# Performance work log

Hardware: AMD Instinct MI355X
Metric: run time of the kernel (lower is better)

## Reference

```python
import jax, jax.numpy as jnp
import numpy as np

LN_EPS = 1e-6


def setup_inputs() -> dict:
    key = jax.random.key(0)
    ks = jax.random.split(key, 3)
    B, S, L, H, V = 16, 512, 2, 1024, 32000
    x = jax.random.randint(ks[0], (B, S), 0, V, dtype=jnp.int64)
    embed = jax.random.normal(ks[1], (V, H), dtype=jnp.float32) * 0.02
    ln_gamma = jnp.ones((L, H), dtype=jnp.float32)
    ln_beta = jnp.zeros((L, H), dtype=jnp.float32)
    W = jax.random.normal(ks[2], (L, 2 * H, 4 * H), dtype=jnp.float32) * (1.0 / np.sqrt(2 * H))
    b = jnp.zeros((L, 4 * H), dtype=jnp.float32)
    return {"x": x, "embed": embed, "ln_gamma": ln_gamma, "ln_beta": ln_beta, "W": W, "b": b}


def _layer_norm(x, g, bt):
    mu = jnp.mean(x, axis=-1, keepdims=True)
    var = jnp.mean(jnp.square(x - mu), axis=-1, keepdims=True)
    return (x - mu) * jax.lax.rsqrt(var + LN_EPS) * g + bt


def reference(x, embed, ln_gamma, ln_beta, W, b):
    L, _, H4 = W.shape
    H = H4 // 4
    B, S = x.shape
    xe = embed[x]  # [B,S,H] token embedding (dropout is identity at eval)

    def step(carry, x_t):
        c, h = carry  # each [L,B,H]
        inp = x_t  # [B,H]
        cs, hs = [], []
        h_out = inp
        for m in range(L):
            xn = _layer_norm(inp, ln_gamma[m], ln_beta[m])
            z = jnp.concatenate([xn, h[m]], axis=-1) @ W[m] + b[m]  # [B,4H]
            zi, zf, zo, zg = z[:, :H], z[:, H:2 * H], z[:, 2 * H:3 * H], z[:, 3 * H:]
            c_new = jax.nn.sigmoid(zf) * c[m] + jax.nn.sigmoid(zi) * jnp.tanh(zg)
            h_new = jax.nn.sigmoid(zo) * jnp.tanh(c_new)
            cs.append(c_new)
            hs.append(h_new)
            h_out = h_new  # raw lstm output of top layer
            inp = h_new + inp  # residual connection feeds next layer
        return (jnp.stack(cs), jnp.stack(hs)), h_out

    c0 = jnp.zeros((L, B, H), dtype=xe.dtype)
    h0 = jnp.zeros((L, B, H), dtype=xe.dtype)
    (c_final, _), h_seq = jax.lax.scan(step, (c0, h0), jnp.transpose(xe, (1, 0, 2)))
    # h_seq: [S,B,H] -> tied-embedding logits [B,S,V]
    logits = jnp.einsum("sbh,vh->bsv", h_seq, embed)
    return c_final, logits
```

## Files before the change

kernel.cpp:

```cpp
#include <hip/hip_runtime.h>
#include <hip/hip_fp16.h>
#include <hip/hip_cooperative_groups.h>

namespace cg = cooperative_groups;

typedef _Float16 f16;
typedef _Float16 f16x8 __attribute__((ext_vector_type(8)));
typedef _Float16 f16x4 __attribute__((ext_vector_type(4)));
typedef float    f32x4 __attribute__((ext_vector_type(4)));

#define LN_EPS 1e-6f

__global__ void k_cvt(const float* __restrict__ in, f16* __restrict__ out, int n4) {
    int i = blockIdx.x * 256 + threadIdx.x;
    int st = gridDim.x * 256;
    for (; i < n4; i += st) {
        float4 v = ((const float4*)in)[i];
        f16x4 o = { (f16)v.x, (f16)v.y, (f16)v.z, (f16)v.w };
        ((f16x4*)out)[i] = o;
    }
}

__global__ void k_xstat(const int* __restrict__ x, const float* __restrict__ embed,
                        float2* __restrict__ xstat) {
    int r = blockIdx.x * 4 + (threadIdx.x >> 6);
    int lane = threadIdx.x & 63;
    int t = r >> 4, b = r & 15;
    int tok = x[b * 512 + t];
    const float4* p = (const float4*)(embed + (size_t)tok * 1024);
    float sum = 0.f, sq = 0.f;
    #pragma unroll
    for (int j = 0; j < 4; ++j) {
        float4 v = p[lane * 4 + j];
        sum += v.x + v.y + v.z + v.w;
        sq  += v.x*v.x + v.y*v.y + v.z*v.z + v.w*v.w;
    }
    #pragma unroll
    for (int m = 1; m < 64; m <<= 1) {
        sum += __shfl_xor(sum, m);
        sq  += __shfl_xor(sq,  m);
    }
    if (lane == 0) {
        float mu  = sum * (1.f / 1024.f);
        float var = sq  * (1.f / 1024.f) - mu * mu;
        xstat[r] = make_float2(mu, rsqrtf(var + LN_EPS));
    }
}

__global__ void __launch_bounds__(256, 1)
k_recur(const int* __restrict__ x, const float* __restrict__ embed,
        const float* __restrict__ gamma, const float* __restrict__ beta,
        const float* __restrict__ W, const float* __restrict__ bias,
        const float2* __restrict__ xstat,
        f16* __restrict__ h0buf, f16* __restrict__ h1buf,
        float* __restrict__ inp1buf,
        f16* __restrict__ hseq,
        float* __restrict__ cout)
{
    extern __shared__ char smem[];
    float* zred  = (float*)(smem + 131072);
    float* stats = (float*)(smem + 131072 + 8192);

    const int tid   = threadIdx.x;
    const int lane  = tid & 63;
    const int wv    = tid >> 6;
    const int blk   = blockIdx.x;
    const int layer = (blk < 128) ? 0 : 1;
    const int base  = (layer ? blk - 128 : blk) * 8;

    {
        const float* Wm = W + (size_t)layer * 2048 * 4096;
        for (int idx = tid; idx < 2048; idx += 256) {
            const int mat = idx >> 10;
            const int k   = idx & 1023;
            const float* row = Wm + (size_t)(mat * 1024 + k) * 4096 + base;
            #pragma unroll
            for (int g = 0; g < 4; ++g) {
                float4 a = *(const float4*)(row + g * 1024);
                float4 c = *(const float4*)(row + g * 1024 + 4);
                float vals[8] = {a.x, a.y, a.z, a.w, c.x, c.y, c.z, c.w};
                #pragma unroll
                for (int u = 0; u < 8; ++u) {
                    int lc  = g * 8 + u;
                    int off = (mat * 65536 + lc * 2048 + k * 2) ^ ((lc & 7) << 4);
                    *(f16*)(smem + off) = (f16)vals[u];
                }
            }
        }
    }

    int grow = 0, gcol = 0;
    float bz0 = 0, bz1 = 0, bz2 = 0, bz3 = 0;
    if (tid < 128) {
        grow = tid >> 3;
        gcol = base + (tid & 7);
        bz0 = bias[layer * 4096 + gcol];
        bz1 = bias[layer * 4096 + 1024 + gcol];
        bz2 = bias[layer * 4096 + 2048 + gcol];
        bz3 = bias[layer * 4096 + 3072 + gcol];
    }
    float creg = 0.f;

    const int arow = lane & 15;
    const int koff = (lane >> 4) * 8;
    const float* gam = gamma + layer * 1024;
    const float* bet = beta  + layer * 1024;

    cg::grid_group grid = cg::this_grid();
    __syncthreads();

    for (int tick = 0; tick <= 512; ++tick) {
        const int  step   = layer ? tick - 1 : tick;
        const bool active = layer ? (tick >= 1) : (tick < 512);
        if (active) {
            if (layer) {
                const float* ip = inp1buf + (step & 1) * (16 * 1024);
                int row = tid >> 4, seg = tid & 15;
                const float4* p = (const float4*)(ip + row * 1024 + seg * 64);
                float sum = 0.f, sq = 0.f;
                #pragma unroll
                for (int j = 0; j < 16; ++j) {
                    float4 v = p[j];
                    sum += v.x + v.y + v.z + v.w;
                    sq  += v.x*v.x + v.y*v.y + v.z*v.z + v.w*v.w;
                }
                #pragma unroll
                for (int m = 1; m < 16; m <<= 1) {
                    sum += __shfl_xor(sum, m);
                    sq  += __shfl_xor(sq,  m);
                }
                if (seg == 0) {
                    float mu  = sum * (1.f / 1024.f);
                    float var = sq  * (1.f / 1024.f) - mu * mu;
                    stats[row * 2]     = mu;
                    stats[row * 2 + 1] = rsqrtf(var + LN_EPS);
                }
                __syncthreads();
            }

            float mu, rsig;
            const float* xrow;
            const f16*   hrow;
            if (layer == 0) {
                int tok = x[arow * 512 + step];
                float2 st = xstat[step * 16 + arow];
                mu = st.x; rsig = st.y;
                xrow = embed + (size_t)tok * 1024;
                hrow = h0buf + ((step + 1) & 1) * (16 * 1024) + arow * 1024;
            } else {
                mu = stats[arow * 2]; rsig = stats[arow * 2 + 1];
                xrow = inp1buf + (step & 1) * (16 * 1024) + arow * 1024;
                hrow = h1buf + ((step + 1) & 1) * (16 * 1024) + arow * 1024;
            }

            f32x4 acc0 = {0.f, 0.f, 0.f, 0.f};
            f32x4 acc1 = {0.f, 0.f, 0.f, 0.f};
            const int lcA = lane & 15;
            #pragma unroll
            for (int ks = 0; ks < 8; ++ks) {
                const int k0 = wv * 256 + ks * 32 + koff;
                float4 e0 = *(const float4*)(xrow + k0);
                float4 e1 = *(const float4*)(xrow + k0 + 4);
                float4 g0 = *(const float4*)(gam + k0);
                float4 g1 = *(const float4*)(gam + k0 + 4);
                float4 q0 = *(const float4*)(bet + k0);
                float4 q1 = *(const float4*)(bet + k0 + 4);
                f16x8 xa;
                xa[0] = (f16)((e0.x - mu) * rsig * g0.x + q0.x);
                xa[1] = (f16)((e0.y - mu) * rsig * g0.y + q0.y);
                xa[2] = (f16)((e0.z - mu) * rsig * g0.z + q0.z);
                xa[3] = (f16)((e0.w - mu) * rsig * g0.w + q0.w);
                xa[4] = (f16)((e1.x - mu) * rsig * g1.x + q1.x);
                xa[5] = (f16)((e1.y - mu) * rsig * g1.y + q1.y);
                xa[6] = (f16)((e1.z - mu) * rsig * g1.z + q1.z);
                xa[7] = (f16)((e1.w - mu) * rsig * g1.w + q1.w);
                f16x8 ha = *(const f16x8*)(hrow + k0);

                int swz0 = (lcA * 2048 + k0 * 2) ^ ((lcA & 7) << 4);
                f16x8 wx0 = *(const f16x8*)(smem + swz0);
                f16x8 wh0 = *(const f16x8*)(smem + 65536 + swz0);
                acc0 = __builtin_amdgcn_mfma_f32_16x16x32_f16(xa, wx0, acc0, 0, 0, 0);
                acc0 = __builtin_amdgcn_mfma_f32_16x16x32_f16(ha, wh0, acc0, 0, 0, 0);
                int lc1  = 16 + lcA;
                int swz1 = (lc1 * 2048 + k0 * 2) ^ ((lc1 & 7) << 4);
                f16x8 wx1 = *(const f16x8*)(smem + swz1);
                f16x8 wh1 = *(const f16x8*)(smem + 65536 + swz1);
                acc1 = __builtin_amdgcn_mfma_f32_16x16x32_f16(xa, wx1, acc1, 0, 0, 0);
                acc1 = __builtin_amdgcn_mfma_f32_16x16x32_f16(ha, wh1, acc1, 0, 0, 0);
            }

            #pragma unroll
            for (int r = 0; r < 4; ++r) {
                int row = (lane >> 4) * 4 + r;
                zred[wv * 512 + row * 32 + (lane & 15)]      = acc0[r];
                zred[wv * 512 + row * 32 + 16 + (lane & 15)] = acc1[r];
            }
            __syncthreads();

            if (tid < 128) {
                int zb = grow * 32 + (tid & 7);
                float zi = bz0, zf = bz1, zo = bz2, zg = bz3;
                #pragma unroll
                for (int w = 0; w < 4; ++w) {
                    zi += zred[w * 512 + zb];
                    zf += zred[w * 512 + zb + 8];
                    zo += zred[w * 512 + zb + 16];
                    zg += zred[w * 512 + zb + 24];
                }
                float si = 1.f / (1.f + expf(-zi));
                float sf = 1.f / (1.f + expf(-zf));
                float so = 1.f / (1.f + expf(-zo));
                float cn = sf * creg + si * tanhf(zg);
                float hn = so * tanhf(cn);
                creg = cn;
                if (layer == 0) {
                    int tok = x[grow * 512 + step];
                    float xe = embed[(size_t)tok * 1024 + gcol];
                    inp1buf[(step & 1) * (16 * 1024) + grow * 1024 + gcol] = hn + xe;
                    h0buf[(step & 1) * (16 * 1024) + grow * 1024 + gcol]   = (f16)hn;
                } else {
                    h1buf[(step & 1) * (16 * 1024) + grow * 1024 + gcol]   = (f16)hn;
                    hseq[((size_t)step * 16 + grow) * 1024 + gcol]          = (f16)hn;
                }
            }
        }
        grid.sync();
    }

    if (tid < 128)
        cout[layer * (16 * 1024) + grow * 1024 + gcol] = creg;
}

__global__ void __launch_bounds__(256)
k_logits(const f16* __restrict__ A, const f16* __restrict__ Bm, float* __restrict__ out) {
    __shared__ f16 Asm[128 * 64];
    __shared__ f16 Bsm[128 * 64];
    const int nwg = gridDim.x;
    int swz = (blockIdx.x % 8) * (nwg / 8) + blockIdx.x / 8;
    const int tm = swz / 250;
    const int tn = swz % 250;
    const int tid = threadIdx.x;
    const int lane = tid & 63;
    const int wv = tid >> 6;
    const int wm = wv >> 1, wn = wv & 1;

    f32x4 acc[4][4] = {};
    const f16* Ab = A  + (size_t)(tm * 128) * 1024;
    const f16* Bb = Bm + (size_t)(tn * 128) * 1024;

    for (int kt = 0; kt < 16; ++kt) {
        uint4 ra[4], rb[4];
        #pragma unroll
        for (int j = 0; j < 4; ++j) {
            int c = tid + j * 256;
            int row = c >> 3, slot = c & 7;
            ra[j] = *(const uint4*)(Ab + (size_t)row * 1024 + kt * 64 + slot * 8);
            rb[j] = *(const uint4*)(Bb + (size_t)row * 1024 + kt * 64 + slot * 8);
        }
        __syncthreads();
        #pragma unroll
        for (int j = 0; j < 4; ++j) {
            int c = tid + j * 256;
            int row = c >> 3, slot = c & 7;
            int off = row * 128 + ((slot ^ (row & 7)) << 4);
            *(uint4*)((char*)Asm + off) = ra[j];
            *(uint4*)((char*)Bsm + off) = rb[j];
        }
        __syncthreads();
        #pragma unroll
        for (int ks = 0; ks < 2; ++ks) {
            f16x8 af[4], bf[4];
            #pragma unroll
            for (int mi = 0; mi < 4; ++mi) {
                int row = wm * 64 + mi * 16 + (lane & 15);
                int slot = ks * 4 + (lane >> 4);
                af[mi] = *(const f16x8*)((const char*)Asm + row * 128 + ((slot ^ (row & 7)) << 4));
            }
            #pragma unroll
            for (int ni = 0; ni < 4; ++ni) {
                int row = wn * 64 + ni * 16 + (lane & 15);
                int slot = ks * 4 + (lane >> 4);
                bf[ni] = *(const f16x8*)((const char*)Bsm + row * 128 + ((slot ^ (row & 7)) << 4));
            }
            #pragma unroll
            for (int mi = 0; mi < 4; ++mi)
                #pragma unroll
                for (int ni = 0; ni < 4; ++ni)
                    acc[mi][ni] = __builtin_amdgcn_mfma_f32_16x16x32_f16(af[mi], bf[ni], acc[mi][ni], 0, 0, 0);
        }
    }

    #pragma unroll
    for (int mi = 0; mi < 4; ++mi) {
        int m16 = tm * 128 + wm * 64 + mi * 16;
        int s = m16 >> 4;
        #pragma unroll
        for (int ni = 0; ni < 4; ++ni) {
            int v = tn * 128 + wn * 64 + ni * 16 + (lane & 15);
            #pragma unroll
            for (int r = 0; r < 4; ++r) {
                int b = (lane >> 4) * 4 + r;
                out[((size_t)b * 512 + s) * 32000 + v] = acc[mi][ni][r];
            }
        }
    }
}

extern "C" void kernel_launch(void* const* d_in, const int* in_sizes, int n_in,
                              void* d_out, int out_size, void* d_ws, size_t ws_size,
                              hipStream_t stream) {
    const int*   x     = (const int*)d_in[0];
    const float* embed = (const float*)d_in[1];
    const float* gamma = (const float*)d_in[2];
    const float* beta  = (const float*)d_in[3];
    const float* W     = (const float*)d_in[4];
    const float* bias  = (const float*)d_in[5];
    float* out = (float*)d_out;

    char* p = (char*)d_ws;
    f16*    embed_f16 = (f16*)p;    p += (size_t)32000 * 1024 * 2;
    f16*    hseq      = (f16*)p;    p += (size_t)512 * 16 * 1024 * 2;
    float2* xstat     = (float2*)p; p += 8192 * 8;
    f16*    h0buf     = (f16*)p;    p += 2 * 16 * 1024 * 2;
    f16*    h1buf     = (f16*)p;    p += 2 * 16 * 1024 * 2;
    float*  inp1buf   = (float*)p;  p += 2 * 16 * 1024 * 4;

    k_cvt<<<2048, 256, 0, stream>>>(embed, embed_f16, 32000 * 1024 / 4);
    k_xstat<<<2048, 256, 0, stream>>>(x, embed, xstat);
    hipMemsetAsync(h0buf, 0, 131072, stream);

    hipFuncSetAttribute((const void*)k_recur,
                        hipFuncAttributeMaxDynamicSharedMemorySize, 139392);
    void* args[] = { (void*)&x, (void*)&embed, (void*)&gamma, (void*)&beta,
                     (void*)&W, (void*)&bias, (void*)&xstat,
                     (void*)&h0buf, (void*)&h1buf, (void*)&inp1buf,
                     (void*)&hseq, (void*)&out };
    hipLaunchCooperativeKernel((const void*)k_recur, dim3(256), dim3(256),
                               args, 139392, stream);

    k_logits<<<16000, 256, 0, stream>>>(hseq, embed_f16, out + 32768);
}
```

Before: 21.73 ms.

## Hoist layer-0 input projection into batched GEMM and replace grid sync with flag barriers

```diff
diff --git a/kernel.cpp b/kernel.cpp
--- a/kernel.cpp
+++ b/kernel.cpp
@@ -1,8 +1,5 @@
 #include <hip/hip_runtime.h>
 #include <hip/hip_fp16.h>
-#include <hip/hip_cooperative_groups.h>
-
-namespace cg = cooperative_groups;
 
 typedef _Float16 f16;
 typedef _Float16 f16x8 __attribute__((ext_vector_type(8)));
@@ -10,6 +7,7 @@
 typedef float    f32x4 __attribute__((ext_vector_type(4)));
 
 #define LN_EPS 1e-6f
+#define AGT __HIP_MEMORY_SCOPE_AGENT
 
 __global__ void k_cvt(const float* __restrict__ in, f16* __restrict__ out, int n4) {
     int i = blockIdx.x * 256 + threadIdx.x;
@@ -47,188 +45,378 @@
     }
 }
 
+__global__ void k_xnorm(const int* __restrict__ x, const float* __restrict__ embed,
+                        const float2* __restrict__ xstat,
+                        const float* __restrict__ gamma, const float* __restrict__ beta,
+                        f16* __restrict__ xn0) {
+    int r = blockIdx.x;
+    int t = r >> 4, b = r & 15;
+    int tok = x[b * 512 + t];
+    int c = threadIdx.x * 4;
+    float4 e = *(const float4*)(embed + (size_t)tok * 1024 + c);
+    float4 g = *(const float4*)(gamma + c);
+    float4 q = *(const float4*)(beta + c);
+    float2 st = xstat[r];
+    f16x4 o;
+    o[0] = (f16)((e.x - st.x) * st.y * g.x + q.x);
+    o[1] = (f16)((e.y - st.x) * st.y * g.y + q.y);
+    o[2] = (f16)((e.z - st.x) * st.y * g.z + q.z);
+    o[3] = (f16)((e.w - st.x) * st.y * g.w + q.w);
+    *(f16x4*)(xn0 + (size_t)r * 1024 + c) = o;
+}
+
+__global__ void k_wprep(const float* __restrict__ W, const float* __restrict__ gamma,
+                        f16* __restrict__ WxT0, f16* __restrict__ WhT0,
+                        f16* __restrict__ WxT1, f16* __restrict__ WhT1) {
+    __shared__ float tile[64][65];
+    int mat = blockIdx.x >> 10, t = blockIdx.x & 1023;
+    int ct = t >> 4, kt = t & 15;
+    int layer = mat >> 1, half = mat & 1;
+    const float* src = W + (size_t)layer * 2048 * 4096 + (size_t)half * 1024 * 4096;
+    int kl = threadIdx.x >> 2, cseg = (threadIdx.x & 3) * 16;
+    float g = (mat == 2) ? gamma[1024 + kt * 64 + kl] : 1.f;
+    const float* srow = src + (size_t)(kt * 64 + kl) * 4096 + ct * 64 + cseg;
+    #pragma unroll
+    for (int j = 0; j < 4; ++j) {
+        float4 v = *(const float4*)(srow + j * 4);
+        tile[kl][cseg + j*4 + 0] = v.x * g;
+        tile[kl][cseg + j*4 + 1] = v.y * g;
+        tile[kl][cseg + j*4 + 2] = v.z * g;
+        tile[kl][cseg + j*4 + 3] = v.w * g;
+    }
+    __syncthreads();
+    f16* dst = (mat == 0) ? WxT0 : (mat == 1) ? WhT0 : (mat == 2) ? WxT1 : WhT1;
+    int cl = threadIdx.x >> 2, kseg = (threadIdx.x & 3) * 16;
+    f16x8 o0, o1;
+    #pragma unroll
+    for (int j = 0; j < 8; ++j) o0[j] = (f16)tile[kseg + j][cl];
+    #pragma unroll
+    for (int j = 0; j < 8; ++j) o1[j] = (f16)tile[kseg + 8 + j][cl];
+    f16* drow = dst + (size_t)(ct * 64 + cl) * 1024 + kt * 64 + kseg;
+    *(f16x8*)drow = o0;
+    *(f16x8*)(drow + 8) = o1;
+}
+
+__global__ void k_gb(const float* __restrict__ W, const float* __restrict__ gamma,
+                     const float* __restrict__ beta,
+                     float* __restrict__ G1, float* __restrict__ Bv1) {
+    int c = blockIdx.x * 256 + threadIdx.x;
+    const float* src = W + (size_t)1 * 2048 * 4096;
+    float G = 0.f, Bv = 0.f;
+    for (int k = 0; k < 1024; ++k) {
+        float w = src[(size_t)k * 4096 + c];
+        G  += gamma[1024 + k] * w;
+        Bv += beta[1024 + k] * w;
+    }
+    G1[c] = G;
+    Bv1[c] = Bv;
+}
+
+__global__ void __launch_bounds__(256)
+k_zx(const f16* __restrict__ A, const f16* __restrict__ Bm, f16* __restrict__ out) {
+    __shared__ f16 Asm[128 * 64];
+    __shared__ f16 Bsm[128 * 64];
+    const int nwg = gridDim.x;
+    int swz = (blockIdx.x % 8) * (nwg / 8) + blockIdx.x / 8;
+    const int tm = swz / 32;
+    const int tn = swz % 32;
+    const int tid = threadIdx.x;
+    const int lane = tid & 63;
+    const int wv = tid >> 6;
+    const int wm = wv >> 1, wn = wv & 1;
+
+    f32x4 acc[4][4] = {};
+    const f16* Ab = A  + (size_t)(tm * 128) * 1024;
+    const f16* Bb = Bm + (size_t)(tn * 128) * 1024;
+
+    for (int kt = 0; kt < 16; ++kt) {
+        uint4 ra[4], rb[4];
+        #pragma unroll
+        for (int j = 0; j < 4; ++j) {
+            int c = tid + j * 256;
+            int row = c >> 3, slot = c & 7;
+            ra[j] = *(const uint4*)(Ab + (size_t)row * 1024 + kt * 64 + slot * 8);
+            rb[j] = *(const uint4*)(Bb + (size_t)row * 1024 + kt * 64 + slot * 8);
+        }
+        __syncthreads();
+        #pragma unroll
+        for (int j = 0; j < 4; ++j) {
+            int c = tid + j * 256;
+            int row = c >> 3, slot = c & 7;
+            int off = row * 128 + ((slot ^ (row & 7)) << 4);
+            *(uint4*)((char*)Asm + off) = ra[j];
+            *(uint4*)((char*)Bsm + off) = rb[j];
+        }
+        __syncthreads();
+        #pragma unroll
+        for (int ks = 0; ks < 2; ++ks) {
+            f16x8 af[4], bf[4];
+            #pragma unroll
+            for (int mi = 0; mi < 4; ++mi) {
+                int row = wm * 64 + mi * 16 + (lane & 15);
+                int slot = ks * 4 + (lane >> 4);
+                af[mi] = *(const f16x8*)((const char*)Asm + row * 128 + ((slot ^ (row & 7)) << 4));
+            }
+            #pragma unroll
+            for (int ni = 0; ni < 4; ++ni) {
+                int row = wn * 64 + ni * 16 + (lane & 15);
+                int slot = ks * 4 + (lane >> 4);
+                bf[ni] = *(const f16x8*)((const char*)Bsm + row * 128 + ((slot ^ (row & 7)) << 4));
+            }
+            #pragma unroll
+            for (int mi = 0; mi < 4; ++mi)
+                #pragma unroll
+                for (int ni = 0; ni < 4; ++ni)
+                    acc[mi][ni] = __builtin_amdgcn_mfma_f32_16x16x32_f16(af[mi], bf[ni], acc[mi][ni], 0, 0, 0);
+        }
+    }
+    #pragma unroll
+    for (int mi = 0; mi < 4; ++mi) {
+        int mrow = tm * 128 + wm * 64 + mi * 16 + (lane >> 4) * 4;
+        #pragma unroll
+        for (int ni = 0; ni < 4; ++ni) {
+            int col = tn * 128 + wn * 64 + ni * 16 + (lane & 15);
+            #pragma unroll
+            for (int r = 0; r < 4; ++r)
+                out[(size_t)(mrow + r) * 4096 + col] = (f16)acc[mi][ni][r];
+        }
+    }
+}
+
+#define GRP 128
 __global__ void __launch_bounds__(256, 1)
 k_recur(const int* __restrict__ x, const float* __restrict__ embed,
-        const float* __restrict__ gamma, const float* __restrict__ beta,
-        const float* __restrict__ W, const float* __restrict__ bias,
-        const float2* __restrict__ xstat,
+        const float* __restrict__ bias,
+        const f16* __restrict__ zx0,
+        const f16* __restrict__ WhT0, const f16* __restrict__ WxT1,
+        const f16* __restrict__ WhT1,
+        const float* __restrict__ G1v, const float* __restrict__ Bv1,
         f16* __restrict__ h0buf, f16* __restrict__ h1buf,
-        float* __restrict__ inp1buf,
+        f16* __restrict__ inp1,
         f16* __restrict__ hseq,
+        unsigned* flags,
         float* __restrict__ cout)
 {
     extern __shared__ char smem[];
     float* zred  = (float*)(smem + 131072);
     float* stats = (float*)(smem + 131072 + 8192);
 
-    const int tid   = threadIdx.x;
-    const int lane  = tid & 63;
-    const int wv    = tid >> 6;
-    const int blk   = blockIdx.x;
-    const int layer = (blk < 128) ? 0 : 1;
-    const int base  = (layer ? blk - 128 : blk) * 8;
-
-    {
-        const float* Wm = W + (size_t)layer * 2048 * 4096;
-        for (int idx = tid; idx < 2048; idx += 256) {
-            const int mat = idx >> 10;
-            const int k   = idx & 1023;
-            const float* row = Wm + (size_t)(mat * 1024 + k) * 4096 + base;
-            #pragma unroll
-            for (int g = 0; g < 4; ++g) {
-                float4 a = *(const float4*)(row + g * 1024);
-                float4 c = *(const float4*)(row + g * 1024 + 4);
-                float vals[8] = {a.x, a.y, a.z, a.w, c.x, c.y, c.z, c.w};
-                #pragma unroll
-                for (int u = 0; u < 8; ++u) {
-                    int lc  = g * 8 + u;
-                    int off = (mat * 65536 + lc * 2048 + k * 2) ^ ((lc & 7) << 4);
-                    *(f16*)(smem + off) = (f16)vals[u];
-                }
-            }
-        }
-    }
-
-    int grow = 0, gcol = 0;
-    float bz0 = 0, bz1 = 0, bz2 = 0, bz3 = 0;
+    const int tid = threadIdx.x;
+    const int lane = tid & 63;
+    const int wv = tid >> 6;
+    const int blk = blockIdx.x;
+    const int layer = blk & 1;
+    const int g = blk >> 1;
+    const int base = g * 8;
+
+    unsigned* arrive    = flags + layer * (GRP * 16);
+    unsigned* progSelf  = flags + 2 * GRP * 16 + layer * 32;
+    unsigned* progOther = flags + 2 * GRP * 16 + (1 - layer) * 32;
+
+    if (layer == 0) {
+        for (int t = tid; t < 4096; t += 256) {
+            int lc = t >> 7, ch = t & 127;
+            int c = (lc >> 3) * 1024 + base + (lc & 7);
+            f16x8 v = *(const f16x8*)(WhT0 + (size_t)c * 1024 + ch * 8);
+            int off = (lc * 2048 + ch * 16) ^ ((lc & 7) << 4);
+            *(f16x8*)(smem + off) = v;
+        }
+        int4* xl = (int4*)(smem + 65536);
+        for (int t = tid; t < 2048; t += 256) xl[t] = ((const int4*)x)[t];
+    } else {
+        for (int t = tid; t < 8192; t += 256) {
+            int mat = t >> 12, r = t & 4095;
+            int lc = r >> 7, ch = r & 127;
+            int c = (lc >> 3) * 1024 + base + (lc & 7);
+            const f16* src = mat ? WhT1 : WxT1;
+            f16x8 v = *(const f16x8*)(src + (size_t)c * 1024 + ch * 8);
+            int off = mat * 65536 + ((lc * 2048 + ch * 16) ^ ((lc & 7) << 4));
+            *(f16x8*)(smem + off) = v;
+        }
+    }
+
+    const int grow = tid >> 3, gu = tid & 7;
+    const int gcol = base + gu;
+    float bz[4], Gg[4], Cg[4];
     if (tid < 128) {
-        grow = tid >> 3;
-        gcol = base + (tid & 7);
-        bz0 = bias[layer * 4096 + gcol];
-        bz1 = bias[layer * 4096 + 1024 + gcol];
-        bz2 = bias[layer * 4096 + 2048 + gcol];
-        bz3 = bias[layer * 4096 + 3072 + gcol];
+        #pragma unroll
+        for (int q = 0; q < 4; ++q) {
+            int cg = q * 1024 + gcol;
+            bz[q] = bias[layer * 4096 + cg];
+            if (layer) { Gg[q] = G1v[cg]; Cg[q] = Bv1[cg] + bz[q]; }
+        }
     }
     float creg = 0.f;
-
     const int arow = lane & 15;
     const int koff = (lane >> 4) * 8;
-    const float* gam = gamma + layer * 1024;
-    const float* bet = beta  + layer * 1024;
-
-    cg::grid_group grid = cg::this_grid();
+    const int lcA = lane & 15;
+
     __syncthreads();
 
-    for (int tick = 0; tick <= 512; ++tick) {
-        const int  step   = layer ? tick - 1 : tick;
-        const bool active = layer ? (tick >= 1) : (tick < 512);
-        if (active) {
-            if (layer) {
-                const float* ip = inp1buf + (step & 1) * (16 * 1024);
-                int row = tid >> 4, seg = tid & 15;
-                const float4* p = (const float4*)(ip + row * 1024 + seg * 64);
-                float sum = 0.f, sq = 0.f;
-                #pragma unroll
-                for (int j = 0; j < 16; ++j) {
-                    float4 v = p[j];
-                    sum += v.x + v.y + v.z + v.w;
-                    sq  += v.x*v.x + v.y*v.y + v.z*v.z + v.w*v.w;
-                }
-                #pragma unroll
-                for (int m = 1; m < 16; m <<= 1) {
-                    sum += __shfl_xor(sum, m);
-                    sq  += __shfl_xor(sq,  m);
-                }
-                if (seg == 0) {
-                    float mu  = sum * (1.f / 1024.f);
-                    float var = sq  * (1.f / 1024.f) - mu * mu;
-                    stats[row * 2]     = mu;
-                    stats[row * 2 + 1] = rsqrtf(var + LN_EPS);
-                }
-                __syncthreads();
-            }
-
-            float mu, rsig;
-            const float* xrow;
-            const f16*   hrow;
-            if (layer == 0) {
-                int tok = x[arow * 512 + step];
-                float2 st = xstat[step * 16 + arow];
-                mu = st.x; rsig = st.y;
-                xrow = embed + (size_t)tok * 1024;
-                hrow = h0buf + ((step + 1) & 1) * (16 * 1024) + arow * 1024;
-            } else {
-                mu = stats[arow * 2]; rsig = stats[arow * 2 + 1];
-                xrow = inp1buf + (step & 1) * (16 * 1024) + arow * 1024;
-                hrow = h1buf + ((step + 1) & 1) * (16 * 1024) + arow * 1024;
-            }
-
-            f32x4 acc0 = {0.f, 0.f, 0.f, 0.f};
-            f32x4 acc1 = {0.f, 0.f, 0.f, 0.f};
-            const int lcA = lane & 15;
+    if (layer == 0) {
+        const int* xtok = (const int*)(smem + 65536);
+        for (int tick = 0; tick < 512; ++tick) {
+            float zx[4]; float xe = 0.f;
+            if (tid < 128) {
+                const f16* zr = zx0 + (size_t)(tick * 16 + grow) * 4096;
+                #pragma unroll
+                for (int q = 0; q < 4; ++q) zx[q] = (float)zr[q * 1024 + gcol];
+                int tok = xtok[grow * 512 + tick];
+                xe = embed[(size_t)tok * 1024 + gcol];
+            }
+            if (tick >= 4) {
+                unsigned tgt = (unsigned)(tick - 3);
+                while (__hip_atomic_load(progOther, __ATOMIC_RELAXED, AGT) < tgt) {}
+            }
+            const f16* hrow = h0buf + ((tick + 1) & 1) * 16384 + arow * 1024;
+            f32x4 acc0 = {0.f,0.f,0.f,0.f}, acc1 = {0.f,0.f,0.f,0.f};
             #pragma unroll
             for (int ks = 0; ks < 8; ++ks) {
-                const int k0 = wv * 256 + ks * 32 + koff;
-                float4 e0 = *(const float4*)(xrow + k0);
-                float4 e1 = *(const float4*)(xrow + k0 + 4);
-                float4 g0 = *(const float4*)(gam + k0);
-                float4 g1 = *(const float4*)(gam + k0 + 4);
-                float4 q0 = *(const float4*)(bet + k0);
-                float4 q1 = *(const float4*)(bet + k0 + 4);
-                f16x8 xa;
-                xa[0] = (f16)((e0.x - mu) * rsig * g0.x + q0.x);
-                xa[1] = (f16)((e0.y - mu) * rsig * g0.y + q0.y);
-                xa[2] = (f16)((e0.z - mu) * rsig * g0.z + q0.z);
-                xa[3] = (f16)((e0.w - mu) * rsig * g0.w + q0.w);
-                xa[4] = (f16)((e1.x - mu) * rsig * g1.x + q1.x);
-                xa[5] = (f16)((e1.y - mu) * rsig * g1.y + q1.y);
-                xa[6] = (f16)((e1.z - mu) * rsig * g1.z + q1.z);
-                xa[7] = (f16)((e1.w - mu) * rsig * g1.w + q1.w);
+                int k0 = wv * 256 + ks * 32 + koff;
                 f16x8 ha = *(const f16x8*)(hrow + k0);
-
                 int swz0 = (lcA * 2048 + k0 * 2) ^ ((lcA & 7) << 4);
-                f16x8 wx0 = *(const f16x8*)(smem + swz0);
-                f16x8 wh0 = *(const f16x8*)(smem + 65536 + swz0);
-                acc0 = __builtin_amdgcn_mfma_f32_16x16x32_f16(xa, wx0, acc0, 0, 0, 0);
-                acc0 = __builtin_amdgcn_mfma_f32_16x16x32_f16(ha, wh0, acc0, 0, 0, 0);
-                int lc1  = 16 + lcA;
+                acc0 = __builtin_amdgcn_mfma_f32_16x16x32_f16(ha, *(const f16x8*)(smem + swz0), acc0, 0, 0, 0);
+                int lc1 = 16 + lcA;
                 int swz1 = (lc1 * 2048 + k0 * 2) ^ ((lc1 & 7) << 4);
-                f16x8 wx1 = *(const f16x8*)(smem + swz1);
-                f16x8 wh1 = *(const f16x8*)(smem + 65536 + swz1);
-                acc1 = __builtin_amdgcn_mfma_f32_16x16x32_f16(xa, wx1, acc1, 0, 0, 0);
-                acc1 = __builtin_amdgcn_mfma_f32_16x16x32_f16(ha, wh1, acc1, 0, 0, 0);
-            }
-
+                acc1 = __builtin_amdgcn_mfma_f32_16x16x32_f16(ha, *(const f16x8*)(smem + swz1), acc1, 0, 0, 0);
+            }
             #pragma unroll
             for (int r = 0; r < 4; ++r) {
                 int row = (lane >> 4) * 4 + r;
-                zred[wv * 512 + row * 32 + (lane & 15)]      = acc0[r];
-                zred[wv * 512 + row * 32 + 16 + (lane & 15)] = acc1[r];
+                zred[wv * 512 + row * 32 + lcA]      = acc0[r];
+                zred[wv * 512 + row * 32 + 16 + lcA] = acc1[r];
             }
             __syncthreads();
-
             if (tid < 128) {
-                int zb = grow * 32 + (tid & 7);
-                float zi = bz0, zf = bz1, zo = bz2, zg = bz3;
-                #pragma unroll
-                for (int w = 0; w < 4; ++w) {
-                    zi += zred[w * 512 + zb];
-                    zf += zred[w * 512 + zb + 8];
-                    zo += zred[w * 512 + zb + 16];
-                    zg += zred[w * 512 + zb + 24];
-                }
+                int zb = grow * 32 + gu;
+                float u[4];
+                #pragma unroll
+                for (int q = 0; q < 4; ++q) {
+                    float s = 0.f;
+                    #pragma unroll
+                    for (int w = 0; w < 4; ++w) s += zred[w * 512 + zb + q * 8];
+                    u[q] = s;
+                }
+                float zi = zx[0] + u[0] + bz[0];
+                float zf = zx[1] + u[1] + bz[1];
+                float zo = zx[2] + u[2] + bz[2];
+                float zg = zx[3] + u[3] + bz[3];
                 float si = 1.f / (1.f + expf(-zi));
                 float sf = 1.f / (1.f + expf(-zf));
                 float so = 1.f / (1.f + expf(-zo));
                 float cn = sf * creg + si * tanhf(zg);
                 float hn = so * tanhf(cn);
                 creg = cn;
-                if (layer == 0) {
-                    int tok = x[grow * 512 + step];
-                    float xe = embed[(size_t)tok * 1024 + gcol];
-                    inp1buf[(step & 1) * (16 * 1024) + grow * 1024 + gcol] = hn + xe;
-                    h0buf[(step & 1) * (16 * 1024) + grow * 1024 + gcol]   = (f16)hn;
-                } else {
-                    h1buf[(step & 1) * (16 * 1024) + grow * 1024 + gcol]   = (f16)hn;
-                    hseq[((size_t)step * 16 + grow) * 1024 + gcol]          = (f16)hn;
-                }
-            }
-        }
-        grid.sync();
+                h0buf[(tick & 1) * 16384 + grow * 1024 + gcol] = (f16)hn;
+                inp1[(tick & 3) * 16384 + grow * 1024 + gcol]  = (f16)(hn + xe);
+            }
+            __syncthreads();
+            if (tid == 0)
+                __hip_atomic_store(&arrive[g * 16], (unsigned)(tick + 1), __ATOMIC_RELEASE, AGT);
+            if (tid < GRP)
+                while (__hip_atomic_load(&arrive[tid * 16], __ATOMIC_RELAXED, AGT) < (unsigned)(tick + 1)) {}
+            __syncthreads();
+            __threadfence();
+            if (g == 0 && tid == 0)
+                __hip_atomic_store(progSelf, (unsigned)(tick + 1), __ATOMIC_RELEASE, AGT);
+        }
+    } else {
+        for (int tick = 1; tick <= 512; ++tick) {
+            const int step = tick - 1;
+            while (__hip_atomic_load(progOther, __ATOMIC_RELAXED, AGT) < (unsigned)tick) {}
+            __threadfence();
+            {
+                int srow = tid >> 4, seg = tid & 15;
+                const f16* p = inp1 + (step & 3) * 16384 + srow * 1024 + seg * 64;
+                float sum = 0.f, sq = 0.f;
+                #pragma unroll
+                for (int j = 0; j < 8; ++j) {
+                    f16x8 v = *(const f16x8*)(p + j * 8);
+                    #pragma unroll
+                    for (int e = 0; e < 8; ++e) { float f = (float)v[e]; sum += f; sq += f * f; }
+                }
+                #pragma unroll
+                for (int m = 1; m < 16; m <<= 1) {
+                    sum += __shfl_xor(sum, m);
+                    sq  += __shfl_xor(sq,  m);
+                }
+                if (seg == 0) {
+                    float mu  = sum * (1.f / 1024.f);
+                    float var = sq * (1.f / 1024.f) - mu * mu;
+                    stats[srow * 2]     = mu;
+                    stats[srow * 2 + 1] = rsqrtf(var + LN_EPS);
+                }
+            }
+            f32x4 acc0 = {0.f,0.f,0.f,0.f}, acc1 = {0.f,0.f,0.f,0.f};
+            if (wv < 2) {
+                const f16* xrow = inp1 + (step & 3) * 16384 + arow * 1024;
+                #pragma unroll
+                for (int ks = 0; ks < 16; ++ks) {
+                    int k0 = wv * 512 + ks * 32 + koff;
+                    f16x8 a = *(const f16x8*)(xrow + k0);
+                    int swz0 = (lcA * 2048 + k0 * 2) ^ ((lcA & 7) << 4);
+                    acc0 = __builtin_amdgcn_mfma_f32_16x16x32_f16(a, *(const f16x8*)(smem + swz0), acc0, 0, 0, 0);
+                    int lc1 = 16 + lcA;
+                    int swz1 = (lc1 * 2048 + k0 * 2) ^ ((lc1 & 7) << 4);
+                    acc1 = __builtin_amdgcn_mfma_f32_16x16x32_f16(a, *(const f16x8*)(smem + swz1), acc1, 0, 0, 0);
+                }
+            } else {
+                const f16* hrow = h1buf + (tick & 1) * 16384 + arow * 1024;
+                #pragma unroll
+                for (int ks = 0; ks < 16; ++ks) {
+                    int k0 = (wv - 2) * 512 + ks * 32 + koff;
+                    f16x8 a = *(const f16x8*)(hrow + k0);
+                    int swz0 = (lcA * 2048 + k0 * 2) ^ ((lcA & 7) << 4);
+                    acc0 = __builtin_amdgcn_mfma_f32_16x16x32_f16(a, *(const f16x8*)(smem + 65536 + swz0), acc0, 0, 0, 0);
+                    int lc1 = 16 + lcA;
+                    int swz1 = (lc1 * 2048 + k0 * 2) ^ ((lc1 & 7) << 4);
+                    acc1 = __builtin_amdgcn_mfma_f32_16x16x32_f16(a, *(const f16x8*)(smem + 65536 + swz1), acc1, 0, 0, 0);
+                }
+            }
+            #pragma unroll
+            for (int r = 0; r < 4; ++r) {
+                int row = (lane >> 4) * 4 + r;
+                zred[wv * 512 + row * 32 + lcA]      = acc0[r];
+                zred[wv * 512 + row * 32 + 16 + lcA] = acc1[r];
+            }
+            __syncthreads();
+            if (tid < 128) {
+                int zb = grow * 32 + gu;
+                float ux[4], uh[4];
+                #pragma unroll
+                for (int q = 0; q < 4; ++q) {
+                    ux[q] = zred[zb + q * 8] + zred[512 + zb + q * 8];
+                    uh[q] = zred[1024 + zb + q * 8] + zred[1536 + zb + q * 8];
+                }
+                float mu = stats[grow * 2], rsig = stats[grow * 2 + 1];
+                float mrs = mu * rsig;
+                float zi = rsig * ux[0] - mrs * Gg[0] + Cg[0] + uh[0];
+                float zf = rsig * ux[1] - mrs * Gg[1] + Cg[1] + uh[1];
+                float zo = rsig * ux[2] - mrs * Gg[2] + Cg[2] + uh[2];
+                float zg = rsig * ux[3] - mrs * Gg[3] + Cg[3] + uh[3];
+                float si = 1.f / (1.f + expf(-zi));
+                float sf = 1.f / (1.f + expf(-zf));
+                float so = 1.f / (1.f + expf(-zo));
+                float cn = sf * creg + si * tanhf(zg);
+                float hn = so * tanhf(cn);
+                creg = cn;
+                h1buf[(step & 1) * 16384 + grow * 1024 + gcol] = (f16)hn;
+                hseq[(size_t)(step * 16 + grow) * 1024 + gcol] = (f16)hn;
+            }
+            __syncthreads();
+            if (tid == 0)
+                __hip_atomic_store(&arrive[g * 16], (unsigned)tick, __ATOMIC_RELEASE, AGT);
+            if (tid < GRP)
+                while (__hip_atomic_load(&arrive[tid * 16], __ATOMIC_RELAXED, AGT) < (unsigned)tick) {}
+            __syncthreads();
+            __threadfence();
+            if (g == 0 && tid == 0)
+                __hip_atomic_store(progSelf, (unsigned)tick, __ATOMIC_RELEASE, AGT);
+        }
     }
 
     if (tid < 128)
-        cout[layer * (16 * 1024) + grow * 1024 + gcol] = creg;
+        cout[layer * 16384 + grow * 1024 + gcol] = creg;
 }
 
 __global__ void __launch_bounds__(256)
@@ -289,7 +477,6 @@
                     acc[mi][ni] = __builtin_amdgcn_mfma_f32_16x16x32_f16(af[mi], bf[ni], acc[mi][ni], 0, 0, 0);
         }
     }
-
     #pragma unroll
     for (int mi = 0; mi < 4; ++mi) {
         int m16 = tm * 128 + wm * 64 + mi * 16;
@@ -318,25 +505,43 @@
     float* out = (float*)d_out;
 
     char* p = (char*)d_ws;
-    f16*    embed_f16 = (f16*)p;    p += (size_t)32000 * 1024 * 2;
-    f16*    hseq      = (f16*)p;    p += (size_t)512 * 16 * 1024 * 2;
-    float2* xstat     = (float2*)p; p += 8192 * 8;
-    f16*    h0buf     = (f16*)p;    p += 2 * 16 * 1024 * 2;
-    f16*    h1buf     = (f16*)p;    p += 2 * 16 * 1024 * 2;
-    float*  inp1buf   = (float*)p;  p += 2 * 16 * 1024 * 4;
-
-    k_cvt<<<2048, 256, 0, stream>>>(embed, embed_f16, 32000 * 1024 / 4);
+    size_t off = 0;
+    f16*      hseq  = (f16*)(p + off);      off += 16777216;
+    float2*   xstat = (float2*)(p + off);   off += 65536;
+    f16*      h0buf = (f16*)(p + off);      off += 65536;
+    f16*      h1buf = (f16*)(p + off);      off += 65536;
+    f16*      inp1  = (f16*)(p + off);      off += 131072;
+    unsigned* flags = (unsigned*)(p + off); off += 16896;
+    size_t xn0_off = off;
+    f16*      xn0   = (f16*)(p + off);      off += 16777216;
+    f16*      WxT0  = (f16*)(p + off);      off += 8388608;
+    f16*      WhT0  = (f16*)(p + off);      off += 8388608;
+    f16*      WxT1  = (f16*)(p + off);      off += 8388608;
+    f16*      WhT1  = (f16*)(p + off);      off += 8388608;
+    float*    G1    = (float*)(p + off);    off += 16384;
+    float*    Bv1   = (float*)(p + off);    off += 16384;
+    f16*      zx0   = (f16*)(p + off);      off += 67108864;
+    f16*      embed_f16 = (f16*)(p + xn0_off);
+
     k_xstat<<<2048, 256, 0, stream>>>(x, embed, xstat);
+    k_xnorm<<<8192, 256, 0, stream>>>(x, embed, xstat, gamma, beta, xn0);
+    k_wprep<<<4096, 256, 0, stream>>>(W, gamma, WxT0, WhT0, WxT1, WhT1);
+    k_gb<<<16, 256, 0, stream>>>(W, gamma, beta, G1, Bv1);
+    k_zx<<<2048, 256, 0, stream>>>(xn0, WxT0, zx0);
+
     hipMemsetAsync(h0buf, 0, 131072, stream);
+    hipMemsetAsync(flags, 0, 16896, stream);
 
     hipFuncSetAttribute((const void*)k_recur,
                         hipFuncAttributeMaxDynamicSharedMemorySize, 139392);
-    void* args[] = { (void*)&x, (void*)&embed, (void*)&gamma, (void*)&beta,
-                     (void*)&W, (void*)&bias, (void*)&xstat,
-                     (void*)&h0buf, (void*)&h1buf, (void*)&inp1buf,
-                     (void*)&hseq, (void*)&out };
+    void* ka[] = { (void*)&x, (void*)&embed, (void*)&bias, (void*)&zx0,
+                   (void*)&WhT0, (void*)&WxT1, (void*)&WhT1,
+                   (void*)&G1, (void*)&Bv1,
+                   (void*)&h0buf, (void*)&h1buf, (void*)&inp1,
+                   (void*)&hseq, (void*)&flags, (void*)&out };
     hipLaunchCooperativeKernel((const void*)k_recur, dim3(256), dim3(256),
-                               args, 139392, stream);
-
+                               ka, 139392, stream);
+
+    k_cvt<<<2048, 256, 0, stream>>>(embed, embed_f16, 32000 * 1024 / 4);
     k_logits<<<16000, 256, 0, stream>>>(hseq, embed_f16, out + 32768);
 }
```

Measured after the change: 24.16 ms. +11.2%, slower.
